# Kernel tuning notes

Measured on AMD Instinct MI355X. Metric: run time of the kernel, lower is better.

## Reference

```python
import jax, jax.numpy as jnp
import numpy as np

DEPTH = 256
SEQ = 394
EMB = 300


def _branch(x_nch, W, b, n):
    # W: [depth, n*EMB], flatten order of paragraph[i:i+n,:].flatten() is (time, emb)
    k = W.reshape(DEPTH, n, EMB).transpose(0, 2, 1)  # OIH: [depth, EMB, n]
    y = jax.lax.conv_general_dilated(
        x_nch, k, window_strides=(1,), padding='VALID',
        dimension_numbers=('NCH', 'OIH', 'NCH'))  # [B, depth, SEQ-n+1]
    # original loop only covers windows i = 0 .. SEQ-n-1 (SEQ-n windows)
    y = y[:, :, :SEQ - n] + b  # b: [depth, 1] broadcasts over time
    # running max starts at 0 and relu clamps >= 0; outer relu is a no-op
    return jnp.max(jax.nn.relu(y), axis=-1)  # [B, depth]


def setup_inputs() -> dict:
    key = jax.random.key(0)
    ks = jax.random.split(key, 7)
    inp = {
        'input': jax.random.normal(ks[0], (64, SEQ, EMB), dtype=jnp.float32),
        'W1': jax.random.normal(ks[1], (DEPTH, 3 * EMB), dtype=jnp.float32),
        'W2': jax.random.normal(ks[2], (DEPTH, 4 * EMB), dtype=jnp.float32),
        'W3': jax.random.normal(ks[3], (DEPTH, 5 * EMB), dtype=jnp.float32),
        'b1': jax.random.normal(ks[4], (DEPTH, 1), dtype=jnp.float32),
        'b2': jax.random.normal(ks[5], (DEPTH, 1), dtype=jnp.float32),
        'b3': jax.random.normal(ks[6], (DEPTH, 1), dtype=jnp.float32),
    }
    return inp


def reference(input, W1, W2, W3, b1, b2, b3):
    x = input.transpose(0, 2, 1)  # [B, EMB, SEQ] (NCH)
    o1 = _branch(x, W1, b1, 3)
    o2 = _branch(x, W2, b2, 4)
    o3 = _branch(x, W3, b3, 5)
    return jnp.concatenate([o1, o2, o3], axis=1)  # [B, 3*depth]
```

## Files before the change

### kernel.cpp

```cpp
#include <hip/hip_runtime.h>
#include <hip/hip_bf16.h>

#define SEQ 394
#define EMB 300
#define EMBP 312
#define NROWS (64 * SEQ)
#define NCHT 118
#define CBE0 29
#define CBE1 68
#define XELEM 41472
#define XGR 5148

typedef __attribute__((ext_vector_type(8))) short short8;
typedef __attribute__((ext_vector_type(4))) float f32x4;

__device__ __forceinline__ unsigned short f2b(float f) {
    unsigned u = __float_as_uint(f);
    u += 0x7FFFu + ((u >> 16) & 1u);
    return (unsigned short)(u >> 16);
}


__global__ __launch_bounds__(256)
void pack_w_kernel(const float* __restrict__ W1, const float* __restrict__ W2,
                   const float* __restrict__ W3, unsigned short* __restrict__ wb)
{
    int G = blockIdx.x * 256 + threadIdx.x;
    int l  = G & 63;
    int g  = (G >> 6) & 15;
    int c  = G >> 10;
    const float* Wg; int n, cb;
    if (c <= CBE0)      { Wg = W1; n = 3; cb = 0;        }
    else if (c <= CBE1) { Wg = W2; n = 4; cb = CBE0 + 1; }
    else                { Wg = W3; n = 5; cb = CBE1 + 1; }
    const int K = n * 300;
    const int f = g * 16 + (l & 15);
    const int kl = (c - cb) * 32 + (l >> 4) * 8;
    unsigned short v[8];
#pragma unroll
    for (int j = 0; j < 8; ++j) {
        int kk = kl + j;
        int r  = kk / EMBP;
        int e  = kk - r * EMBP;
        v[j] = (r < n && e < 300) ? f2b(Wg[(long)f * K + r * 300 + e]) : (unsigned short)0;
    }
    unsigned short* dst = wb + (long)G * 8;
    *(ushort4*)dst       = make_ushort4(v[0], v[1], v[2], v[3]);
    *(ushort4*)(dst + 4) = make_ushort4(v[4], v[5], v[6], v[7]);
}


__global__ __launch_bounds__(1024, 1)
void convgemm_kernel(const float* __restrict__ x,
                     const unsigned short* __restrict__ wb,
                     const float* __restrict__ b1, const float* __restrict__ b2,
                     const float* __restrict__ b3,
                     float* __restrict__ out)
{
    __shared__ unsigned short X[XELEM];

    const int tid  = threadIdx.x;
    const int lane = tid & 63;
    const int wid  = tid >> 6;
    const int wfs  = wid >> 1;
    const int ws   = wid & 1;
    const int lr   = lane & 15, lg = lane >> 4;
    const int b    = blockIdx.x >> 2;
    const int ti   = blockIdx.x & 3;
    const int woff = (ti == 0) ? 0 : (ti == 1) ? 88 : (ti == 2) ? 176 : 263;

    const unsigned short* wp0 = wb + ((long)(wfs * 2) * 64 + lane) * 8;
    auto LDW = [&](int c, short8 (&w)[2]) {
        const short8* p = (const short8*)(wp0 + (long)c * 8192);
        w[0] = p[0];
        w[1] = p[64];
    };

    short8 w1[2], w2[2];
    LDW(30, w1); LDW(69, w2);

    {
        const float* xs = x + ((long)b * SEQ + woff) * 300;
        const long growbase = (long)b * SEQ + woff;
#pragma unroll
        for (int rd = 0; rd < 6; ++rd) {
            int gi = rd * 1024 + tid;
            if (gi < XGR) {
                int row = gi / 39;
                int g   = gi - row * 39;
                const float* src = xs + (long)gi * 8 - 12 * row;
                float4 v0 = make_float4(0.f, 0.f, 0.f, 0.f);
                float4 v1 = make_float4(0.f, 0.f, 0.f, 0.f);
                if (growbase + row < NROWS) {
                    if (g < 37) {
                        v0 = *(const float4*)src;
                        v1 = *(const float4*)(src + 4);
                    } else if (g == 37) {
                        v0 = *(const float4*)src;
                    }
                }
                *(ushort4*)&X[gi * 8]     = make_ushort4(f2b(v0.x), f2b(v0.y), f2b(v0.z), f2b(v0.w));
                *(ushort4*)&X[gi * 8 + 4] = make_ushort4(f2b(v1.x), f2b(v1.y), f2b(v1.z), f2b(v1.w));
            }
        }
    }
    __syncthreads();

    const unsigned short* xr = &X[(ws * 64 + lr) * EMBP + lg * 8];
    auto RDBX = [&](int ko, short8 (&bx)[4]) {
        bx[0] = *(const short8*)(xr + ko);
        bx[1] = *(const short8*)(xr + ko + 16 * EMBP);
        bx[2] = *(const short8*)(xr + ko + 32 * EMBP);
        bx[3] = *(const short8*)(xr + ko + 48 * EMBP);
    };

    auto MFMA8 = [&](const short8 (&w)[2], const short8 (&bx)[4], f32x4 (&acc)[2][4]) {
#pragma unroll
        for (int mi = 0; mi < 2; ++mi)
#pragma unroll
            for (int ni = 0; ni < 4; ++ni)
                acc[mi][ni] = __builtin_amdgcn_mfma_f32_16x16x32_bf16(w[mi], bx[ni], acc[mi][ni], 0, 0, 0);
    };

    auto EPI = [&](int br, f32x4 (&acc)[2][4]) {
        const float* bg = (br == 0) ? b1 : (br == 1) ? b2 : b3;
        const int Nw = 391 - br;
        const int ob = b * 768 + br * 256;
#pragma unroll
        for (int mi = 0; mi < 2; ++mi) {
#pragma unroll
            for (int r = 0; r < 4; ++r) {
                const int d = wfs * 32 + mi * 16 + lg * 4 + r;
                const float bv = bg[d];
                float m = 0.f;
#pragma unroll
                for (int ni = 0; ni < 4; ++ni) {
                    int w = woff + ws * 64 + ni * 16 + lr;
                    float v = fmaxf(acc[mi][ni][r] + bv, 0.f);
                    if (w >= Nw) v = 0.f;
                    m = fmaxf(m, v);
                }
#pragma unroll
                for (int off = 1; off < 16; off <<= 1)
                    m = fmaxf(m, __shfl_xor(m, off));
                if (lr == 0)
                    atomicMax((int*)(out + ob + d), __float_as_int(m));
            }
        }
#pragma unroll
        for (int i = 0; i < 2; ++i)
#pragma unroll
            for (int j = 0; j < 4; ++j)
                acc[i][j] = (f32x4)0.0f;
    };

    f32x4 accA[2][4], accB[2][4];
#pragma unroll
    for (int i = 0; i < 2; ++i)
#pragma unroll
        for (int j = 0; j < 4; ++j) {
            accA[i][j] = (f32x4)0.0f;
            accB[i][j] = (f32x4)0.0f;
        }

    short8 bxA[4], bxB[4];
    RDBX(0, bxA);

    for (int j = 0; j < 38; j += 2) {
        RDBX((j + 1) * 32, bxB);
        __builtin_amdgcn_sched_barrier(0);
        __builtin_amdgcn_s_setprio(1);
        MFMA8(w1, bxA, accA);
        MFMA8(w2, bxA, accB);
        __builtin_amdgcn_s_setprio(0);
        LDW(30 + j + 1, w1); LDW(69 + j + 1, w2);

        RDBX((j + 2) * 32, bxA);
        __builtin_amdgcn_sched_barrier(0);
        __builtin_amdgcn_s_setprio(1);
        MFMA8(w1, bxB, accA);
        MFMA8(w2, bxB, accB);
        __builtin_amdgcn_s_setprio(0);
        LDW(30 + j + 2, w1); LDW(69 + j + 2, w2);
    }
    __builtin_amdgcn_s_setprio(1);
    MFMA8(w1, bxA, accA);
    MFMA8(w2, bxA, accB);
    __builtin_amdgcn_s_setprio(0);

    LDW(108, w2);
    RDBX(39 * 32, bxB);
    EPI(1, accA);

    for (int u = 0; u < 10; u += 2) {
        RDBX((40 + u) * 32, bxA);
        __builtin_amdgcn_sched_barrier(0);
        __builtin_amdgcn_s_setprio(1);
        MFMA8(w2, bxB, accB);
        __builtin_amdgcn_s_setprio(0);
        LDW(109 + u, w2);

        { int t = (41 + u <= 48) ? 41 + u : 48; RDBX(t * 32, bxB); }
        __builtin_amdgcn_sched_barrier(0);
        __builtin_amdgcn_s_setprio(1);
        MFMA8(w2, bxA, accB);
        __builtin_amdgcn_s_setprio(0);
        { int t = (110 + u <= 117) ? 110 + u : 117; LDW(t, w2); }
    }

    LDW(0, w1);
    RDBX(0, bxA);
    EPI(2, accB);

    for (int j = 0; j < 30; j += 2) {
        RDBX((j + 1) * 32, bxB);
        __builtin_amdgcn_sched_barrier(0);
        __builtin_amdgcn_s_setprio(1);
        MFMA8(w1, bxA, accA);
        __builtin_amdgcn_s_setprio(0);
        LDW(j + 1, w1);

        { int t = (j + 2 <= 29) ? j + 2 : 29; RDBX(t * 32, bxA); }
        __builtin_amdgcn_sched_barrier(0);
        __builtin_amdgcn_s_setprio(1);
        MFMA8(w1, bxB, accA);
        __builtin_amdgcn_s_setprio(0);
        { int t = (j + 2 <= 29) ? j + 2 : 29; LDW(t, w1); }
    }
    EPI(0, accA);
}


__device__ __forceinline__ void load_chunk(const float* __restrict__ Wg,
                                           const float* __restrict__ xb,
                                           int K, int dbase, int i0, int k0, int tid,
                                           float4 wv[4], float4 xv[4])
{
#pragma unroll
    for (int i = 0; i < 4; ++i) {
        int fi  = tid + (i << 8);
        int row = fi >> 3;
        int c4  = (fi & 7) << 2;
        int col = k0 + c4;
        if (col < K)
            wv[i] = *(const float4*)(Wg + (long)(dbase + row) * K + col);
        else
            wv[i] = make_float4(0.f, 0.f, 0.f, 0.f);
        int off = (i0 + row) * EMB + col;
        int lim = SEQ * EMB - 4;
        if (off > lim) off = lim;
        xv[i] = *(const float4*)(xb + off);
    }
}

__device__ __forceinline__ void write_chunk(unsigned short (*Wb)[40],
                                            unsigned short (*Xb)[40],
                                            int tid, const float4 wv[4], const float4 xv[4])
{
#pragma unroll
    for (int i = 0; i < 4; ++i) {
        int fi  = tid + (i << 8);
        int row = fi >> 3;
        int c4  = (fi & 7) << 2;
        *(ushort4*)&Wb[row][c4] = make_ushort4(f2b(wv[i].x), f2b(wv[i].y), f2b(wv[i].z), f2b(wv[i].w));
        *(ushort4*)&Xb[row][c4] = make_ushort4(f2b(xv[i].x), f2b(xv[i].y), f2b(xv[i].z), f2b(xv[i].w));
    }
}

__global__ __launch_bounds__(256, 2)
void convmax_fallback(const float* __restrict__ x,
                      const float* __restrict__ W1, const float* __restrict__ W2,
                      const float* __restrict__ W3,
                      const float* __restrict__ b1, const float* __restrict__ b2,
                      const float* __restrict__ b3,
                      float* __restrict__ out)
{
    const int br = blockIdx.z;
    const int K  = (br == 0) ? 900 : (br == 1) ? 1200 : 1500;
    const int Nw = SEQ - 3 - br;
    const float* Wg = (br == 0) ? W1 : (br == 1) ? W2 : W3;
    const float* bg = (br == 0) ? b1 : (br == 1) ? b2 : b3;
    const int b  = blockIdx.x;
    const int mt = blockIdx.y >> 2;
    const int nt = blockIdx.y & 3;
    const int dbase = mt * 128;
    const int i0    = nt * 128;
    const float* xb = x + b * (SEQ * EMB);
    const int nch = (K + 31) >> 5;

    __shared__ unsigned short Wl[2][128][40];
    __shared__ unsigned short Xl[2][128][40];

    const int tid  = threadIdx.x;
    const int lane = tid & 63;
    const int wid  = tid >> 6;
    const int wr = wid >> 1, wc = wid & 1;
    const int lr = lane & 15, lg = lane >> 4;

    f32x4 acc[4][4];
#pragma unroll
    for (int i = 0; i < 4; ++i)
#pragma unroll
        for (int j = 0; j < 4; ++j)
            acc[i][j] = (f32x4)0.0f;

    {
        float4 wv[4], xv[4];
        load_chunk(Wg, xb, K, dbase, i0, 0, tid, wv, xv);
        write_chunk(Wl[0], Xl[0], tid, wv, xv);
    }
    __syncthreads();

    for (int c = 0; c < nch; ++c) {
        const int cur = c & 1;
        float4 wv[4], xv[4];
        const bool pf = (c + 1 < nch);
        if (pf) load_chunk(Wg, xb, K, dbase, i0, (c + 1) << 5, tid, wv, xv);

        short8 af[4], bfr[4];
#pragma unroll
        for (int mi = 0; mi < 4; ++mi)
            af[mi] = *(const short8*)&Wl[cur][wr * 64 + mi * 16 + lr][lg * 8];
#pragma unroll
        for (int ni = 0; ni < 4; ++ni)
            bfr[ni] = *(const short8*)&Xl[cur][wc * 64 + ni * 16 + lr][lg * 8];
#pragma unroll
        for (int mi = 0; mi < 4; ++mi)
#pragma unroll
            for (int ni = 0; ni < 4; ++ni)
                acc[mi][ni] = __builtin_amdgcn_mfma_f32_16x16x32_bf16(af[mi], bfr[ni], acc[mi][ni], 0, 0, 0);

        if (pf) write_chunk(Wl[cur ^ 1], Xl[cur ^ 1], tid, wv, xv);
        __syncthreads();
    }

    const int ob = b * 768 + br * 256;
#pragma unroll
    for (int mi = 0; mi < 4; ++mi) {
#pragma unroll
        for (int rI = 0; rI < 4; ++rI) {
            const int d = dbase + wr * 64 + mi * 16 + lg * 4 + rI;
            const float bv = bg[d];
            float m = 0.f;
#pragma unroll
            for (int ni = 0; ni < 4; ++ni) {
                int win = i0 + wc * 64 + ni * 16 + lr;
                float v = acc[mi][ni][rI] + bv;
                v = fmaxf(v, 0.f);
                if (win >= Nw) v = 0.f;
                m = fmaxf(m, v);
            }
#pragma unroll
            for (int off = 1; off < 16; off <<= 1)
                m = fmaxf(m, __shfl_xor(m, off));
            if (lr == 0)
                atomicMax((int*)(out + ob + d), __float_as_int(m));
        }
    }
}


extern "C" void kernel_launch(void* const* d_in, const int* in_sizes, int n_in,
                              void* d_out, int out_size, void* d_ws, size_t ws_size,
                              hipStream_t stream) {
    const float* x  = (const float*)d_in[0];
    const float* W1 = (const float*)d_in[1];
    const float* W2 = (const float*)d_in[2];
    const float* W3 = (const float*)d_in[3];
    const float* b1 = (const float*)d_in[4];
    const float* b2 = (const float*)d_in[5];
    const float* b3 = (const float*)d_in[6];
    float* out = (float*)d_out;

    hipMemsetAsync(d_out, 0, (size_t)out_size * sizeof(float), stream);

    const size_t need = (size_t)NCHT * 8192 * 2;

    if (ws_size >= need) {
        unsigned short* wbb = (unsigned short*)d_ws;
        pack_w_kernel<<<472, 256, 0, stream>>>(W1, W2, W3, wbb);
        convgemm_kernel<<<256, 1024, 0, stream>>>(x, wbb, b1, b2, b3, out);
    } else {
        dim3 grid(64, 8, 3);
        convmax_fallback<<<grid, 256, 0, stream>>>(x, W1, W2, W3, b1, b2, b3, out);
    }
}
```

Baseline: 80.61 us.

## Split conv GEMM into smaller 512-thread blocks with overlapping window tiles

Each batch is now split into eight 64-window tiles at stride 49 instead of four 128-window tiles, so each block runs 512 threads with half the LDS. Launch bounds allow several blocks per CU to improve latency hiding. The change also drops the explicit sched_barrier and setprio hints and writes each LDS group with one 16-byte store. In exchange, overlapping tiles repeat some MFMA work, and each block streams the full weight set, so weight traffic doubles.

After: 81.25 us. About the same (+0.8%).

```diff
diff --git a/kernel.cpp b/kernel.cpp
--- a/kernel.cpp
+++ b/kernel.cpp
@@ -8,8 +8,9 @@
 #define NCHT 118
 #define CBE0 29
 #define CBE1 68
-#define XELEM 41472
-#define XGR 5148
+#define XROWS 69
+#define XGR 2691
+#define XELEM 21528
 
 typedef __attribute__((ext_vector_type(8))) short short8;
 typedef __attribute__((ext_vector_type(4))) float f32x4;
@@ -50,7 +51,7 @@
 }
 
 
-__global__ __launch_bounds__(1024, 1)
+__global__ __launch_bounds__(512, 4)
 void convgemm_kernel(const float* __restrict__ x,
                      const unsigned short* __restrict__ wb,
                      const float* __restrict__ b1, const float* __restrict__ b2,
@@ -61,13 +62,11 @@
 
     const int tid  = threadIdx.x;
     const int lane = tid & 63;
-    const int wid  = tid >> 6;
-    const int wfs  = wid >> 1;
-    const int ws   = wid & 1;
+    const int wfs  = tid >> 6;
     const int lr   = lane & 15, lg = lane >> 4;
-    const int b    = blockIdx.x >> 2;
-    const int ti   = blockIdx.x & 3;
-    const int woff = (ti == 0) ? 0 : (ti == 1) ? 88 : (ti == 2) ? 176 : 263;
+    const int b    = blockIdx.x >> 3;
+    const int ti   = blockIdx.x & 7;
+    const int woff = ti * 49;
 
     const unsigned short* wp0 = wb + ((long)(wfs * 2) * 64 + lane) * 8;
     auto LDW = [&](int c, short8 (&w)[2]) {
@@ -84,7 +83,7 @@
         const long growbase = (long)b * SEQ + woff;
 #pragma unroll
         for (int rd = 0; rd < 6; ++rd) {
-            int gi = rd * 1024 + tid;
+            int gi = rd * 512 + tid;
             if (gi < XGR) {
                 int row = gi / 39;
                 int g   = gi - row * 39;
@@ -99,14 +98,18 @@
                         v0 = *(const float4*)src;
                     }
                 }
-                *(ushort4*)&X[gi * 8]     = make_ushort4(f2b(v0.x), f2b(v0.y), f2b(v0.z), f2b(v0.w));
-                *(ushort4*)&X[gi * 8 + 4] = make_ushort4(f2b(v1.x), f2b(v1.y), f2b(v1.z), f2b(v1.w));
+                short8 s;
+                s[0] = (short)f2b(v0.x); s[1] = (short)f2b(v0.y);
+                s[2] = (short)f2b(v0.z); s[3] = (short)f2b(v0.w);
+                s[4] = (short)f2b(v1.x); s[5] = (short)f2b(v1.y);
+                s[6] = (short)f2b(v1.z); s[7] = (short)f2b(v1.w);
+                *(short8*)&X[gi * 8] = s;
             }
         }
     }
     __syncthreads();
 
-    const unsigned short* xr = &X[(ws * 64 + lr) * EMBP + lg * 8];
+    const unsigned short* xr = &X[lr * EMBP + lg * 8];
     auto RDBX = [&](int ko, short8 (&bx)[4]) {
         bx[0] = *(const short8*)(xr + ko);
         bx[1] = *(const short8*)(xr + ko + 16 * EMBP);
@@ -135,7 +138,7 @@
                 float m = 0.f;
 #pragma unroll
                 for (int ni = 0; ni < 4; ++ni) {
-                    int w = woff + ws * 64 + ni * 16 + lr;
+                    int w = woff + ni * 16 + lr;
                     float v = fmaxf(acc[mi][ni][r] + bv, 0.f);
                     if (w >= Nw) v = 0.f;
                     m = fmaxf(m, v);
@@ -168,25 +171,17 @@
 
     for (int j = 0; j < 38; j += 2) {
         RDBX((j + 1) * 32, bxB);
-        __builtin_amdgcn_sched_barrier(0);
-        __builtin_amdgcn_s_setprio(1);
         MFMA8(w1, bxA, accA);
         MFMA8(w2, bxA, accB);
-        __builtin_amdgcn_s_setprio(0);
         LDW(30 + j + 1, w1); LDW(69 + j + 1, w2);
 
         RDBX((j + 2) * 32, bxA);
-        __builtin_amdgcn_sched_barrier(0);
-        __builtin_amdgcn_s_setprio(1);
         MFMA8(w1, bxB, accA);
         MFMA8(w2, bxB, accB);
-        __builtin_amdgcn_s_setprio(0);
         LDW(30 + j + 2, w1); LDW(69 + j + 2, w2);
     }
-    __builtin_amdgcn_s_setprio(1);
     MFMA8(w1, bxA, accA);
     MFMA8(w2, bxA, accB);
-    __builtin_amdgcn_s_setprio(0);
 
     LDW(108, w2);
     RDBX(39 * 32, bxB);
@@ -194,17 +189,11 @@
 
     for (int u = 0; u < 10; u += 2) {
         RDBX((40 + u) * 32, bxA);
-        __builtin_amdgcn_sched_barrier(0);
-        __builtin_amdgcn_s_setprio(1);
         MFMA8(w2, bxB, accB);
-        __builtin_amdgcn_s_setprio(0);
         LDW(109 + u, w2);
 
         { int t = (41 + u <= 48) ? 41 + u : 48; RDBX(t * 32, bxB); }
-        __builtin_amdgcn_sched_barrier(0);
-        __builtin_amdgcn_s_setprio(1);
         MFMA8(w2, bxA, accB);
-        __builtin_amdgcn_s_setprio(0);
         { int t = (110 + u <= 117) ? 110 + u : 117; LDW(t, w2); }
     }
 
@@ -214,17 +203,11 @@
 
     for (int j = 0; j < 30; j += 2) {
         RDBX((j + 1) * 32, bxB);
-        __builtin_amdgcn_sched_barrier(0);
-        __builtin_amdgcn_s_setprio(1);
         MFMA8(w1, bxA, accA);
-        __builtin_amdgcn_s_setprio(0);
         LDW(j + 1, w1);
 
         { int t = (j + 2 <= 29) ? j + 2 : 29; RDBX(t * 32, bxA); }
-        __builtin_amdgcn_sched_barrier(0);
-        __builtin_amdgcn_s_setprio(1);
         MFMA8(w1, bxB, accA);
-        __builtin_amdgcn_s_setprio(0);
         { int t = (j + 2 <= 29) ? j + 2 : 29; LDW(t, w1); }
     }
     EPI(0, accA);
@@ -379,7 +362,7 @@
     if (ws_size >= need) {
         unsigned short* wbb = (unsigned short*)d_ws;
         pack_w_kernel<<<472, 256, 0, stream>>>(W1, W2, W3, wbb);
-        convgemm_kernel<<<256, 1024, 0, stream>>>(x, wbb, b1, b2, b3, out);
+        convgemm_kernel<<<512, 512, 0, stream>>>(x, wbb, b1, b2, b3, out);
     } else {
         dim3 grid(64, 8, 3);
         convmax_fallback<<<grid, 256, 0, stream>>>(x, W1, W2, W3, b1, b2, b3, out);
```
